# Kernel optimization log

Hardware: AMD Instinct MI355X
Metric: run time of the kernel (lower is better)

Reference implementation:

```python
import jax, jax.numpy as jnp
import numpy as np

N = 10000   # num_nodes
E = 320000  # num_edges (avg degree 32)
IN, HID, OUT = 512, 512, 256


def setup_inputs() -> dict:
    key = jax.random.key(0)
    ks = jax.random.split(key, 19)
    rn = lambda k, shape: (jax.random.normal(k, shape, jnp.float32) * 0.05)
    edge_index = jax.random.randint(ks[0], (2, E), 0, N, dtype=jnp.int32)
    return {
        "edge_index": edge_index,
        "w_pe": rn(ks[1], (IN, N)), "b_pe": rn(ks[2], (IN,)),
        "w_self0": rn(ks[3], (HID, IN)), "w_neigh0": rn(ks[4], (HID, IN)), "b0": rn(ks[5], (HID,)),
        "w_res0": rn(ks[6], (HID, IN)), "rb0": rn(ks[7], (HID,)),
        "w_self1": rn(ks[8], (HID, HID)), "w_neigh1": rn(ks[9], (HID, HID)), "b1": rn(ks[10], (HID,)),
        "w_res1": rn(ks[11], (HID, HID)), "rb1": rn(ks[12], (HID,)),
        "w_self2": rn(ks[13], (OUT, HID)), "w_neigh2": rn(ks[14], (OUT, HID)), "b2": rn(ks[15], (OUT,)),
        "w_res2": rn(ks[16], (OUT, HID)), "rb2": rn(ks[17], (OUT,)),
    }


def reference(edge_index, w_pe, b_pe,
              w_self0, w_neigh0, b0, w_res0, rb0,
              w_self1, w_neigh1, b1, w_res1, rb1,
              w_self2, w_neigh2, b2, w_res2, rb2):
    src, dst = edge_index[0], edge_index[1]

    def mean_agg(h):
        # mean of neighbor features per destination node (sparse SAGE aggregation)
        s = jax.ops.segment_sum(h[src], dst, num_segments=N)           # [N, D]
        deg = jax.ops.segment_sum(jnp.ones((E,), h.dtype), dst, num_segments=N)
        return s / jnp.maximum(deg, 1.0)[:, None]

    # pe = Linear(eye(N)) as in the original module
    pe = jnp.eye(N, dtype=w_pe.dtype) @ w_pe.T + b_pe                   # [N, IN]

    layers = [
        (w_self0, w_neigh0, b0, w_res0, rb0),
        (w_self1, w_neigh1, b1, w_res1, rb1),
        (w_self2, w_neigh2, b2, w_res2, rb2),
    ]

    h = pe
    mids = []
    for i, (ws, wn, b, wr, rb) in enumerate(layers):
        h_prev = h
        # SAGEConv (mean): fc_self(h) + fc_neigh(mean_neigh(h))
        h = h @ ws.T + mean_agg(h_prev) @ wn.T + b
        if i != len(layers) - 1:
            h = jax.nn.leaky_relu(h, 0.01)
            # F.dropout with training=False is identity (inference reference)
        h = h + (h_prev @ wr.T + rb)  # residual linear
        mids.append(h)
    return (h, *mids)
```

## Files before the change

### kernel.cpp

```cpp
#include <hip/hip_runtime.h>

#define N_NODES 10000
#define N_EDGES 320000
#define DIN 512
#define DHID 512
#define DOUT 256

typedef __bf16 bf16x8 __attribute__((ext_vector_type(8)));
typedef float f32x4 __attribute__((ext_vector_type(4)));
typedef unsigned short ushort_t;
typedef unsigned int uint_t;

__device__ __forceinline__ float b2f(ushort_t u){
    union { uint_t i; float f; } v; v.i = (uint_t)u << 16; return v.f;
}
__device__ __forceinline__ float blo(uint_t v){
    union { uint_t i; float f; } u; u.i = v << 16; return u.f;
}
__device__ __forceinline__ float bhi(uint_t v){
    union { uint_t i; float f; } u; u.i = v & 0xffff0000u; return u.f;
}
__device__ __forceinline__ ushort_t f2b(float f){
    union { float f; uint_t i; } v; v.f = f;
    uint_t i = v.i;
    return (ushort_t)((i + 0x7fffu + ((i >> 16) & 1u)) >> 16);
}

__device__ __forceinline__ void gll16(const ushort_t* g, ushort_t* l){
    __builtin_amdgcn_global_load_lds(
        (const __attribute__((address_space(1))) unsigned int*)g,
        (__attribute__((address_space(3))) unsigned int*)l,
        16, 0, 0);
}


__global__ void k_degree(const int* __restrict__ dst, int* __restrict__ deg){
    int e = blockIdx.x * 256 + threadIdx.x;
    if (e < N_EDGES) atomicAdd(&deg[dst[e]], 1);
}

__global__ void k_scan(const int* __restrict__ deg, int* __restrict__ row_ptr,
                       int* __restrict__ cursor){
    __shared__ int part[256];
    int t = threadIdx.x;
    int base = t * 40;
    int loc[40];
    int s = 0;
    #pragma unroll
    for (int i = 0; i < 40; ++i){
        int idx = base + i;
        int v = (idx < N_NODES) ? deg[idx] : 0;
        s += v; loc[i] = s;
    }
    part[t] = s;
    __syncthreads();
    int val = s;
    for (int off = 1; off < 256; off <<= 1){
        int x = (t >= off) ? part[t - off] : 0;
        __syncthreads();
        val += x; part[t] = val;
        __syncthreads();
    }
    int exc = val - s;
    if (t == 0) row_ptr[0] = 0;
    int run = exc;
    #pragma unroll
    for (int i = 0; i < 40; ++i){
        int idx = base + i;
        if (idx < N_NODES){
            row_ptr[idx + 1] = exc + loc[i];
            cursor[idx] = run;
        }
        run = exc + loc[i];
    }
}

__global__ void k_scatter(const int* __restrict__ src, const int* __restrict__ dst,
                          int* __restrict__ cursor, int* __restrict__ srcs){
    int e = blockIdx.x * 256 + threadIdx.x;
    if (e < N_EDGES){
        int p = atomicAdd(&cursor[dst[e]], 1);
        srcs[p] = src[e];
    }
}


struct CvtArgs { const float* s[8]; const float* s2[8]; ushort_t* d[8]; int n[8]; };

__global__ void k_pro(const float* __restrict__ w_pe, const float* __restrict__ b_pe,
                      ushort_t* __restrict__ h0, CvtArgs a,
                      int* __restrict__ deg, uint_t* __restrict__ zp){
    __shared__ float lt[64][68];
    int bid = blockIdx.x;
    int t = threadIdx.x;
    if (bid < 1256){
        int n0 = (bid % 157) * 64, i0 = (bid / 157) * 64;
        int nc = (t & 15) * 4, ir = t >> 4;
        #pragma unroll
        for (int p = 0; p < 4; ++p){
            int i_loc = ir + p * 16;
            float4 v = {0.f, 0.f, 0.f, 0.f};
            if (n0 + nc < N_NODES)
                v = *(const float4*)&w_pe[(size_t)(i0 + i_loc) * N_NODES + n0 + nc];
            lt[nc + 0][i_loc] = v.x;
            lt[nc + 1][i_loc] = v.y;
            lt[nc + 2][i_loc] = v.z;
            lt[nc + 3][i_loc] = v.w;
        }
        __syncthreads();
        int ic = t & 7, nr = t >> 3;
        #pragma unroll
        for (int p = 0; p < 2; ++p){
            int n_loc = nr + p * 32;
            int n = n0 + n_loc;
            if (n < N_NODES){
                uint4 u;
                u.x = (uint_t)f2b(lt[n_loc][ic*8+0] + b_pe[i0+ic*8+0])
                    | ((uint_t)f2b(lt[n_loc][ic*8+1] + b_pe[i0+ic*8+1]) << 16);
                u.y = (uint_t)f2b(lt[n_loc][ic*8+2] + b_pe[i0+ic*8+2])
                    | ((uint_t)f2b(lt[n_loc][ic*8+3] + b_pe[i0+ic*8+3]) << 16);
                u.z = (uint_t)f2b(lt[n_loc][ic*8+4] + b_pe[i0+ic*8+4])
                    | ((uint_t)f2b(lt[n_loc][ic*8+5] + b_pe[i0+ic*8+5]) << 16);
                u.w = (uint_t)f2b(lt[n_loc][ic*8+6] + b_pe[i0+ic*8+6])
                    | ((uint_t)f2b(lt[n_loc][ic*8+7] + b_pe[i0+ic*8+7]) << 16);
                *(uint4*)&h0[(size_t)n * DIN + i0 + ic * 8] = u;
            }
        }
    } else if (bid < 2280){
        int j = bid - 1256;
        int m = j >> 7;
        int i = (((j & 127) * 256) + t) * 8;
        if (i < a.n[m]){
            const float* sp = a.s[m] + i;
            float4 f0 = *(const float4*)sp;
            float4 f1 = *(const float4*)(sp + 4);
            if (a.s2[m]){
                const float* sq = a.s2[m] + i;
                float4 g0 = *(const float4*)sq;
                float4 g1 = *(const float4*)(sq + 4);
                f0.x += g0.x; f0.y += g0.y; f0.z += g0.z; f0.w += g0.w;
                f1.x += g1.x; f1.y += g1.y; f1.z += g1.z; f1.w += g1.w;
            }
            uint4 u;
            u.x = (uint_t)f2b(f0.x) | ((uint_t)f2b(f0.y) << 16);
            u.y = (uint_t)f2b(f0.z) | ((uint_t)f2b(f0.w) << 16);
            u.z = (uint_t)f2b(f1.x) | ((uint_t)f2b(f1.y) << 16);
            u.w = (uint_t)f2b(f1.z) | ((uint_t)f2b(f1.w) << 16);
            *(uint4*)&a.d[m][i] = u;
        }
    } else {
        int i = (bid - 2280) * 256 + t;
        if (i < N_NODES) deg[i] = 0;
        if (i < 256) zp[i] = 0u;
    }
}


#define AGG_EDGE(e, CH) { \
    int s_ = __builtin_amdgcn_readlane(sr, (e)); \
    uint_t v_ = *(const uint_t*)&X[((size_t)(uint_t)s_ << 9) + col]; \
    CH##0 += blo(v_); CH##1 += bhi(v_); }

__global__ __launch_bounds__(256) void k_agg(
    const ushort_t* __restrict__ X, const int* __restrict__ row_ptr,
    const int* __restrict__ srcs, ushort_t* __restrict__ out, int dummy)
{
    int w = threadIdx.x >> 6, lane = threadIdx.x & 63;
    int n = blockIdx.x * 4 + w;
    int col = blockIdx.y * 128 + lane * 2;
    int beg = row_ptr[n], end = row_ptr[n + 1];
    int deg = end - beg;
    float a0=0.f,a1=0.f, p0=0.f,p1=0.f, c0=0.f,c1=0.f, d0=0.f,d1=0.f;

    for (int base = beg; base < end; base += 64){
        int rem = end - base;
        int sr = (lane < rem) ? srcs[base + lane] : dummy;
        int cnt = rem < 64 ? rem : 64;
        #pragma unroll
        for (int k = 0; k < 4; ++k){
            if (k * 16 < cnt){
                int L = k * 16;
                AGG_EDGE(L + 0,  a) AGG_EDGE(L + 1,  p) AGG_EDGE(L + 2,  c) AGG_EDGE(L + 3,  d)
                AGG_EDGE(L + 4,  a) AGG_EDGE(L + 5,  p) AGG_EDGE(L + 6,  c) AGG_EDGE(L + 7,  d)
                AGG_EDGE(L + 8,  a) AGG_EDGE(L + 9,  p) AGG_EDGE(L + 10, c) AGG_EDGE(L + 11, d)
                AGG_EDGE(L + 12, a) AGG_EDGE(L + 13, p) AGG_EDGE(L + 14, c) AGG_EDGE(L + 15, d)
            }
        }
    }

    float r0 = (a0 + p0) + (c0 + d0);
    float r1 = (a1 + p1) + (c1 + d1);
    float inv = (deg > 0) ? 1.f / (float)deg : 1.f;
    uint_t o = (uint_t)f2b(r0 * inv) | ((uint_t)f2b(r1 * inv) << 16);
    *(uint_t*)&out[(size_t)n * 512 + col] = o;
}


#define AGGF_EDGE(e, CH) { \
    int s_ = __builtin_amdgcn_readlane(sr, (e)); \
    uint_t v_ = *(const uint_t*)&P[((size_t)(uint_t)s_ << 8) + col]; \
    CH##0 += blo(v_); CH##1 += bhi(v_); }

__global__ __launch_bounds__(256) void k_aggf(
    const ushort_t* __restrict__ P, const int* __restrict__ row_ptr,
    const int* __restrict__ srcs, const float* __restrict__ Q,
    float* __restrict__ fin, float* __restrict__ mid2, int dummy)
{
    int w = threadIdx.x >> 6, lane = threadIdx.x & 63;
    int n = blockIdx.x * 4 + w;
    int col = blockIdx.y * 128 + lane * 2;
    int beg = row_ptr[n], end = row_ptr[n + 1];
    int deg = end - beg;
    float a0=0.f,a1=0.f, p0=0.f,p1=0.f, c0=0.f,c1=0.f, d0=0.f,d1=0.f;

    for (int base = beg; base < end; base += 64){
        int rem = end - base;
        int sr = (lane < rem) ? srcs[base + lane] : dummy;
        int cnt = rem < 64 ? rem : 64;
        #pragma unroll
        for (int k = 0; k < 4; ++k){
            if (k * 16 < cnt){
                int L = k * 16;
                AGGF_EDGE(L + 0,  a) AGGF_EDGE(L + 1,  p) AGGF_EDGE(L + 2,  c) AGGF_EDGE(L + 3,  d)
                AGGF_EDGE(L + 4,  a) AGGF_EDGE(L + 5,  p) AGGF_EDGE(L + 6,  c) AGGF_EDGE(L + 7,  d)
                AGGF_EDGE(L + 8,  a) AGGF_EDGE(L + 9,  p) AGGF_EDGE(L + 10, c) AGGF_EDGE(L + 11, d)
                AGGF_EDGE(L + 12, a) AGGF_EDGE(L + 13, p) AGGF_EDGE(L + 14, c) AGGF_EDGE(L + 15, d)
            }
        }
    }

    float r0 = (a0 + p0) + (c0 + d0);
    float r1 = (a1 + p1) + (c1 + d1);
    float inv = (deg > 0) ? 1.f / (float)deg : 1.f;
    float2 q = *(const float2*)&Q[(size_t)n * 256 + col];
    float2 o;
    o.x = q.x + r0 * inv;
    o.y = q.y + r1 * inv;
    *(float2*)&fin [(size_t)n * 256 + col] = o;
    *(float2*)&mid2[(size_t)n * 256 + col] = o;
}


template<int DO, int BN, bool ACT, bool WRITE_BF>
__global__ __launch_bounds__(256, 2) void k_layer(
    const ushort_t* __restrict__ X, const ushort_t* __restrict__ G,
    const ushort_t* __restrict__ Ws, const ushort_t* __restrict__ Wn,
    const ushort_t* __restrict__ Wr,
    const float* __restrict__ b, const float* __restrict__ rb,
    float* __restrict__ Y, ushort_t* __restrict__ YB)
{
    constexpr int BM   = 160;
    constexpr int NT   = DO / BN;
    constexpr int WTN  = BN / 32;
    constexpr int NCH  = (2 * BM + 3 * BN) / 16;
    constexpr int CHPW = (NCH + 3) / 4;
    constexpr int OG   = BM * 32;
    constexpr int OS   = 2 * BM * 32;
    constexpr int WS32 = BN * 32;
    constexpr int BUFSZ = OS + 3 * WS32;
    __shared__ __align__(16) ushort_t smem[2][BUFSZ];

    int t = threadIdx.x;
    int bid = blockIdx.x;
    int r8 = bid & 7, q8 = bid >> 3;
    int m_t = (q8 / NT) * 8 + r8;
    int n_t = q8 % NT;
    if (m_t * BM >= N_NODES) return;
    int m0 = m_t * BM, n0 = n_t * BN;

    int lane = t & 63, w = t >> 6;
    int wr = w >> 1, wc = w & 1;

    const ushort_t* gptr[CHPW];
    int coff[CHPW];
    bool gv[CHPW];
    int rl = lane >> 2;
    int sl = ((lane & 3) ^ ((rl >> 1) & 3)) * 8;
    #pragma unroll
    for (int i = 0; i < CHPW; ++i){
        int qq = w * CHPW + i;
        gv[i] = (qq < NCH);
        int qc = gv[i] ? qq : 0;
        const ushort_t* gA; int rowbase, off;
        if (qc < 10)      { gA = X;  rowbase = m0 + qc * 16;        off = qc * 512; }
        else if (qc < 20) { gA = G;  rowbase = m0 + (qc - 10) * 16; off = OG + (qc - 10) * 512; }
        else {
            int q2 = qc - 20;
            int sec = q2 / (BN / 16), wi = q2 % (BN / 16);
            gA = (sec == 0) ? Ws : (sec == 1) ? Wn : Wr;
            rowbase = n0 + wi * 16;
            off = OS + sec * WS32 + wi * 512;
        }
        gptr[i] = gA + (size_t)(rowbase + rl) * 512 + sl;
        coff[i] = off;
    }

    f32x4 accS[5][WTN] = {}, accG[5][WTN] = {}, accR[5][WTN] = {};
    int r16 = lane & 15;
    int arow = wr * 80 + r16;
    int brow = wc * (BN / 2) + r16;
    int kk = ((lane >> 4) ^ ((r16 >> 1) & 3)) * 8;

    #pragma unroll
    for (int i = 0; i < CHPW; ++i) if (gv[i]) gll16(gptr[i], &smem[0][coff[i]]);
    __syncthreads();

    int cur = 0;
    for (int ks = 0; ks < 16; ++ks){
        if (ks < 15){
            int k0 = (ks + 1) * 32;
            #pragma unroll
            for (int i = 0; i < CHPW; ++i) if (gv[i]) gll16(gptr[i] + k0, &smem[cur ^ 1][coff[i]]);
        }

        const ushort_t* sb = smem[cur];
        bf16x8 ax[5], ag[5], bs[WTN], bn_[WTN], brr[WTN];
        #pragma unroll
        for (int m = 0; m < 5; ++m){
            ax[m] = *(const bf16x8*)&sb[(arow + m * 16) * 32 + kk];
            ag[m] = *(const bf16x8*)&sb[OG + (arow + m * 16) * 32 + kk];
        }
        #pragma unroll
        for (int n = 0; n < WTN; ++n){
            bs[n]  = *(const bf16x8*)&sb[OS            + (brow + n * 16) * 32 + kk];
            bn_[n] = *(const bf16x8*)&sb[OS + WS32     + (brow + n * 16) * 32 + kk];
            brr[n] = *(const bf16x8*)&sb[OS + 2 * WS32 + (brow + n * 16) * 32 + kk];
        }
        #pragma unroll
        for (int m = 0; m < 5; ++m)
            #pragma unroll
            for (int n = 0; n < WTN; ++n){
                accS[m][n] = __builtin_amdgcn_mfma_f32_16x16x32_bf16(ax[m], bs[n],  accS[m][n], 0, 0, 0);
                accG[m][n] = __builtin_amdgcn_mfma_f32_16x16x32_bf16(ag[m], bn_[n], accG[m][n], 0, 0, 0);
                accR[m][n] = __builtin_amdgcn_mfma_f32_16x16x32_bf16(ax[m], brr[n], accR[m][n], 0, 0, 0);
            }

        __syncthreads();
        cur ^= 1;
    }

    int col_l = lane & 15;
    int row_l = (lane >> 4) * 4;
    #pragma unroll
    for (int n = 0; n < WTN; ++n){
        int col = n0 + wc * (BN / 2) + n * 16 + col_l;
        float bb = b[col], rbb = rb[col];
        #pragma unroll
        for (int m = 0; m < 5; ++m){
            #pragma unroll
            for (int j = 0; j < 4; ++j){
                int row = m0 + wr * 80 + m * 16 + row_l + j;
                if (row < N_NODES){
                    float v = accS[m][n][j] + accG[m][n][j] + bb;
                    if (ACT) v = (v > 0.f) ? v : 0.01f * v;
                    v += accR[m][n][j] + rbb;
                    Y[(size_t)row * DO + col] = v;
                    if (WRITE_BF) YB[(size_t)row * DO + col] = f2b(v);
                }
            }
        }
    }
}


__global__ __launch_bounds__(256, 2) void k_layer2(
    const ushort_t* __restrict__ X,
    const ushort_t* __restrict__ Wn, const ushort_t* __restrict__ Wsr,
    const float* __restrict__ b, const float* __restrict__ rb,
    ushort_t* __restrict__ Pout, float* __restrict__ Qout)
{
    constexpr int BM = 160, BN = 32, NT = DOUT / BN;
    constexpr int NCH = 10 + 2 * (BN / 16);
    constexpr int CHPW = 4;
    constexpr int OWN = BM * 32;
    constexpr int OWS = OWN + BN * 32;
    constexpr int BUFSZ = OWS + BN * 32;
    __shared__ __align__(16) ushort_t smem[2][BUFSZ];

    int t = threadIdx.x;
    int bid = blockIdx.x;
    int r8 = bid & 7, q8 = bid >> 3;
    int m_t = (q8 / NT) * 8 + r8;
    int n_t = q8 % NT;
    if (m_t * BM >= N_NODES) return;
    int m0 = m_t * BM, n0 = n_t * BN;

    int lane = t & 63, w = t >> 6;
    int wr = w >> 1, wc = w & 1;

    const ushort_t* gptr[CHPW];
    int coff[CHPW];
    bool gv[CHPW];
    int rl = lane >> 2;
    int sl = ((lane & 3) ^ ((rl >> 1) & 3)) * 8;
    #pragma unroll
    for (int i = 0; i < CHPW; ++i){
        int qq = w * CHPW + i;
        gv[i] = (qq < NCH);
        int qc = gv[i] ? qq : 0;
        const ushort_t* gA; int rowbase, off;
        if (qc < 10)      { gA = X;   rowbase = m0 + qc * 16;        off = qc * 512; }
        else if (qc < 12) { gA = Wn;  rowbase = n0 + (qc - 10) * 16; off = OWN + (qc - 10) * 512; }
        else              { gA = Wsr; rowbase = n0 + (qc - 12) * 16; off = OWS + (qc - 12) * 512; }
        gptr[i] = gA + (size_t)(rowbase + rl) * 512 + sl;
        coff[i] = off;
    }

    f32x4 accP[5] = {}, accQ[5] = {};
    int r16 = lane & 15;
    int arow = wr * 80 + r16;
    int brow = wc * 16 + r16;
    int kk = ((lane >> 4) ^ ((r16 >> 1) & 3)) * 8;

    #pragma unroll
    for (int i = 0; i < CHPW; ++i) if (gv[i]) gll16(gptr[i], &smem[0][coff[i]]);
    __syncthreads();

    int cur = 0;
    for (int ks = 0; ks < 16; ++ks){
        if (ks < 15){
            int k0 = (ks + 1) * 32;
            #pragma unroll
            for (int i = 0; i < CHPW; ++i) if (gv[i]) gll16(gptr[i] + k0, &smem[cur ^ 1][coff[i]]);
        }

        const ushort_t* sb = smem[cur];
        bf16x8 ax[5];
        #pragma unroll
        for (int m = 0; m < 5; ++m)
            ax[m] = *(const bf16x8*)&sb[(arow + m * 16) * 32 + kk];
        bf16x8 bn_ = *(const bf16x8*)&sb[OWN + brow * 32 + kk];
        bf16x8 bsr = *(const bf16x8*)&sb[OWS + brow * 32 + kk];
        #pragma unroll
        for (int m = 0; m < 5; ++m){
            accP[m] = __builtin_amdgcn_mfma_f32_16x16x32_bf16(ax[m], bn_, accP[m], 0, 0, 0);
            accQ[m] = __builtin_amdgcn_mfma_f32_16x16x32_bf16(ax[m], bsr, accQ[m], 0, 0, 0);
        }

        __syncthreads();
        cur ^= 1;
    }

    int col_l = lane & 15;
    int row_l = (lane >> 4) * 4;
    int col = n0 + wc * 16 + col_l;
    float bb = b[col] + rb[col];
    #pragma unroll
    for (int m = 0; m < 5; ++m){
        #pragma unroll
        for (int j = 0; j < 4; ++j){
            int row = m0 + wr * 80 + m * 16 + row_l + j;
            if (row < N_NODES){
                Qout[(size_t)row * DOUT + col] = accQ[m][j] + bb;
                Pout[(size_t)row * DOUT + col] = f2b(accP[m][j]);
            }
        }
    }
}


extern "C" void kernel_launch(void* const* d_in, const int* in_sizes, int n_in,
                              void* d_out, int out_size, void* d_ws, size_t ws_size,
                              hipStream_t stream) {
    const int* edge  = (const int*)d_in[0];
    const int* e_src = edge;
    const int* e_dst = edge + N_EDGES;
    const float* w_pe = (const float*)d_in[1];
    const float* b_pe = (const float*)d_in[2];
    const float* ws0 = (const float*)d_in[3];
    const float* wn0 = (const float*)d_in[4];
    const float* b0  = (const float*)d_in[5];
    const float* wr0 = (const float*)d_in[6];
    const float* rb0 = (const float*)d_in[7];
    const float* ws1 = (const float*)d_in[8];
    const float* wn1 = (const float*)d_in[9];
    const float* b1  = (const float*)d_in[10];
    const float* wr1 = (const float*)d_in[11];
    const float* rb1 = (const float*)d_in[12];
    const float* ws2 = (const float*)d_in[13];
    const float* wn2 = (const float*)d_in[14];
    const float* b2  = (const float*)d_in[15];
    const float* wr2 = (const float*)d_in[16];
    const float* rb2 = (const float*)d_in[17];

    char* wsb = (char*)d_ws;
    ushort_t* h0   = (ushort_t*)wsb;
    ushort_t* hb   = (ushort_t*)(wsb + 10240000);
    ushort_t* aggb = (ushort_t*)(wsb + 20480000);
    ushort_t* wbf  = (ushort_t*)(wsb + 30720000);
    int* deg     = (int*)(wsb + 34652160);
    int* row_ptr = deg + 10016;
    int* cursor  = row_ptr + 10016;
    int* srcs    = cursor + 10016;
    uint_t* zp   = (uint_t*)(wsb + 36052992);
    const int dummy_h0 = 35208;
    const int dummy_hb = 25208;
    const int dummy_pb = 30416;

    ushort_t* wbf0s = wbf;
    ushort_t* wbf0n = wbf + 262144;
    ushort_t* wbf0r = wbf + 524288;
    ushort_t* wbf1s = wbf + 786432;
    ushort_t* wbf1n = wbf + 1048576;
    ushort_t* wbf1r = wbf + 1310720;
    ushort_t* wbf2n = wbf + 1572864;
    ushort_t* wbf2sr= wbf + 1703936;

    float* out  = (float*)d_out;
    float* fin  = out;
    float* mid0 = out + 2560000;
    float* mid1 = out + 7680000;
    float* mid2 = out + 12800000;
    ushort_t* pb = aggb;

    CvtArgs ca;
    ca.s[0]=ws0; ca.s[1]=wn0; ca.s[2]=wr0;
    ca.s[3]=ws1; ca.s[4]=wn1; ca.s[5]=wr1;
    ca.s[6]=wn2; ca.s[7]=ws2;
    for (int i = 0; i < 8; ++i) ca.s2[i] = nullptr;
    ca.s2[7] = wr2;
    ca.d[0]=wbf0s; ca.d[1]=wbf0n; ca.d[2]=wbf0r;
    ca.d[3]=wbf1s; ca.d[4]=wbf1n; ca.d[5]=wbf1r;
    ca.d[6]=wbf2n; ca.d[7]=wbf2sr;
    for (int i = 0; i < 6; ++i) ca.n[i] = 262144;
    ca.n[6] = 131072; ca.n[7] = 131072;

    k_pro<<<2320, 256, 0, stream>>>(w_pe, b_pe, h0, ca, deg, zp);

    k_degree <<<1250, 256, 0, stream>>>(e_dst, deg);
    k_scan   <<<1, 256, 0, stream>>>(deg, row_ptr, cursor);
    k_scatter<<<1250, 256, 0, stream>>>(e_src, e_dst, cursor, srcs);

    k_agg<<<dim3(2500, 4), 256, 0, stream>>>(h0, row_ptr, srcs, aggb, dummy_h0);
    k_layer<512, 64, true, true ><<<dim3(512), 256, 0, stream>>>(
        h0, aggb, wbf0s, wbf0n, wbf0r, b0, rb0, mid0, hb);

    k_agg<<<dim3(2500, 4), 256, 0, stream>>>(hb, row_ptr, srcs, aggb, dummy_hb);
    k_layer<512, 64, true, true ><<<dim3(512), 256, 0, stream>>>(
        hb, aggb, wbf1s, wbf1n, wbf1r, b1, rb1, mid1, h0);

    k_layer2<<<dim3(512), 256, 0, stream>>>(h0, wbf2n, wbf2sr, b2, rb2, pb, mid2);
    k_aggf<<<dim3(2500, 2), 256, 0, stream>>>(pb, row_ptr, srcs, mid2, fin, mid2, dummy_pb);
}
```

Measured before the change: 206.5 us.

## Merge prologue and CSR build into one cooperative kernel with grid syncs

Folds four front-end kernels (weight conversion and PE transpose, degree count, scan, scatter) into one persistent cooperative kernel of 1024 blocks. Grid-wide syncs separate the phases. The aim is to remove three kernel launch gaps and the tail drain between them. In exchange, the single-block scan phase now leaves the rest of the grid idle at a barrier, and a cooperative launch needs all 1024 blocks to be co-resident.

```diff
diff --git a/kernel.cpp b/kernel.cpp
--- a/kernel.cpp
+++ b/kernel.cpp
@@ -1,4 +1,7 @@
 #include <hip/hip_runtime.h>
+#include <hip/hip_cooperative_groups.h>
+
+namespace cg = cooperative_groups;
 
 #define N_NODES 10000
 #define N_EDGES 320000
@@ -34,124 +37,133 @@
 }
 
 
-__global__ void k_degree(const int* __restrict__ dst, int* __restrict__ deg){
-    int e = blockIdx.x * 256 + threadIdx.x;
-    if (e < N_EDGES) atomicAdd(&deg[dst[e]], 1);
-}
-
-__global__ void k_scan(const int* __restrict__ deg, int* __restrict__ row_ptr,
-                       int* __restrict__ cursor){
-    __shared__ int part[256];
+struct CvtArgs { const float* s[8]; const float* s2[8]; ushort_t* d[8]; int n[8]; };
+
+__global__ void k_front(const int* __restrict__ e_src, const int* __restrict__ e_dst,
+                        const float* __restrict__ w_pe, const float* __restrict__ b_pe,
+                        ushort_t* __restrict__ h0, CvtArgs a,
+                        int* __restrict__ deg, uint_t* __restrict__ zp,
+                        int* __restrict__ row_ptr, int* __restrict__ cursor,
+                        int* __restrict__ srcs){
+    cg::grid_group grid = cg::this_grid();
+    __shared__ float lt[64][68];
     int t = threadIdx.x;
-    int base = t * 40;
-    int loc[40];
-    int s = 0;
-    #pragma unroll
-    for (int i = 0; i < 40; ++i){
-        int idx = base + i;
-        int v = (idx < N_NODES) ? deg[idx] : 0;
-        s += v; loc[i] = s;
-    }
-    part[t] = s;
-    __syncthreads();
-    int val = s;
-    for (int off = 1; off < 256; off <<= 1){
-        int x = (t >= off) ? part[t - off] : 0;
+
+    for (int job = blockIdx.x; job < 2320; job += gridDim.x){
+        if (job < 1256){
+            int n0 = (job % 157) * 64, i0 = (job / 157) * 64;
+            int nc = (t & 15) * 4, ir = t >> 4;
+            #pragma unroll
+            for (int p = 0; p < 4; ++p){
+                int i_loc = ir + p * 16;
+                float4 v = {0.f, 0.f, 0.f, 0.f};
+                if (n0 + nc < N_NODES)
+                    v = *(const float4*)&w_pe[(size_t)(i0 + i_loc) * N_NODES + n0 + nc];
+                lt[nc + 0][i_loc] = v.x;
+                lt[nc + 1][i_loc] = v.y;
+                lt[nc + 2][i_loc] = v.z;
+                lt[nc + 3][i_loc] = v.w;
+            }
+            __syncthreads();
+            int ic = t & 7, nr = t >> 3;
+            #pragma unroll
+            for (int p = 0; p < 2; ++p){
+                int n_loc = nr + p * 32;
+                int n = n0 + n_loc;
+                if (n < N_NODES){
+                    uint4 u;
+                    u.x = (uint_t)f2b(lt[n_loc][ic*8+0] + b_pe[i0+ic*8+0])
+                        | ((uint_t)f2b(lt[n_loc][ic*8+1] + b_pe[i0+ic*8+1]) << 16);
+                    u.y = (uint_t)f2b(lt[n_loc][ic*8+2] + b_pe[i0+ic*8+2])
+                        | ((uint_t)f2b(lt[n_loc][ic*8+3] + b_pe[i0+ic*8+3]) << 16);
+                    u.z = (uint_t)f2b(lt[n_loc][ic*8+4] + b_pe[i0+ic*8+4])
+                        | ((uint_t)f2b(lt[n_loc][ic*8+5] + b_pe[i0+ic*8+5]) << 16);
+                    u.w = (uint_t)f2b(lt[n_loc][ic*8+6] + b_pe[i0+ic*8+6])
+                        | ((uint_t)f2b(lt[n_loc][ic*8+7] + b_pe[i0+ic*8+7]) << 16);
+                    *(uint4*)&h0[(size_t)n * DIN + i0 + ic * 8] = u;
+                }
+            }
+        } else if (job < 2280){
+            int j = job - 1256;
+            int m = j >> 7;
+            int i = (((j & 127) * 256) + t) * 8;
+            if (i < a.n[m]){
+                const float* sp = a.s[m] + i;
+                float4 f0 = *(const float4*)sp;
+                float4 f1 = *(const float4*)(sp + 4);
+                if (a.s2[m]){
+                    const float* sq = a.s2[m] + i;
+                    float4 g0 = *(const float4*)sq;
+                    float4 g1 = *(const float4*)(sq + 4);
+                    f0.x += g0.x; f0.y += g0.y; f0.z += g0.z; f0.w += g0.w;
+                    f1.x += g1.x; f1.y += g1.y; f1.z += g1.z; f1.w += g1.w;
+                }
+                uint4 u;
+                u.x = (uint_t)f2b(f0.x) | ((uint_t)f2b(f0.y) << 16);
+                u.y = (uint_t)f2b(f0.z) | ((uint_t)f2b(f0.w) << 16);
+                u.z = (uint_t)f2b(f1.x) | ((uint_t)f2b(f1.y) << 16);
+                u.w = (uint_t)f2b(f1.z) | ((uint_t)f2b(f1.w) << 16);
+                *(uint4*)&a.d[m][i] = u;
+            }
+        } else {
+            int i = (job - 2280) * 256 + t;
+            if (i < N_NODES) deg[i] = 0;
+            if (i < 256) zp[i] = 0u;
+        }
         __syncthreads();
-        val += x; part[t] = val;
+    }
+    __threadfence();
+    grid.sync();
+
+    for (int job = blockIdx.x; job < 1250; job += gridDim.x){
+        int e = job * 256 + t;
+        if (e < N_EDGES) atomicAdd(&deg[e_dst[e]], 1);
+    }
+    __threadfence();
+    grid.sync();
+
+    if (blockIdx.x == 0){
+        int* part = (int*)&lt[0][0];
+        int base = t * 40;
+        int loc[40];
+        int s = 0;
+        #pragma unroll
+        for (int i = 0; i < 40; ++i){
+            int idx = base + i;
+            int v = (idx < N_NODES) ? deg[idx] : 0;
+            s += v; loc[i] = s;
+        }
+        part[t] = s;
         __syncthreads();
-    }
-    int exc = val - s;
-    if (t == 0) row_ptr[0] = 0;
-    int run = exc;
-    #pragma unroll
-    for (int i = 0; i < 40; ++i){
-        int idx = base + i;
-        if (idx < N_NODES){
-            row_ptr[idx + 1] = exc + loc[i];
-            cursor[idx] = run;
-        }
-        run = exc + loc[i];
-    }
-}
-
-__global__ void k_scatter(const int* __restrict__ src, const int* __restrict__ dst,
-                          int* __restrict__ cursor, int* __restrict__ srcs){
-    int e = blockIdx.x * 256 + threadIdx.x;
-    if (e < N_EDGES){
-        int p = atomicAdd(&cursor[dst[e]], 1);
-        srcs[p] = src[e];
-    }
-}
-
-
-struct CvtArgs { const float* s[8]; const float* s2[8]; ushort_t* d[8]; int n[8]; };
-
-__global__ void k_pro(const float* __restrict__ w_pe, const float* __restrict__ b_pe,
-                      ushort_t* __restrict__ h0, CvtArgs a,
-                      int* __restrict__ deg, uint_t* __restrict__ zp){
-    __shared__ float lt[64][68];
-    int bid = blockIdx.x;
-    int t = threadIdx.x;
-    if (bid < 1256){
-        int n0 = (bid % 157) * 64, i0 = (bid / 157) * 64;
-        int nc = (t & 15) * 4, ir = t >> 4;
-        #pragma unroll
-        for (int p = 0; p < 4; ++p){
-            int i_loc = ir + p * 16;
-            float4 v = {0.f, 0.f, 0.f, 0.f};
-            if (n0 + nc < N_NODES)
-                v = *(const float4*)&w_pe[(size_t)(i0 + i_loc) * N_NODES + n0 + nc];
-            lt[nc + 0][i_loc] = v.x;
-            lt[nc + 1][i_loc] = v.y;
-            lt[nc + 2][i_loc] = v.z;
-            lt[nc + 3][i_loc] = v.w;
-        }
-        __syncthreads();
-        int ic = t & 7, nr = t >> 3;
-        #pragma unroll
-        for (int p = 0; p < 2; ++p){
-            int n_loc = nr + p * 32;
-            int n = n0 + n_loc;
-            if (n < N_NODES){
-                uint4 u;
-                u.x = (uint_t)f2b(lt[n_loc][ic*8+0] + b_pe[i0+ic*8+0])
-                    | ((uint_t)f2b(lt[n_loc][ic*8+1] + b_pe[i0+ic*8+1]) << 16);
-                u.y = (uint_t)f2b(lt[n_loc][ic*8+2] + b_pe[i0+ic*8+2])
-                    | ((uint_t)f2b(lt[n_loc][ic*8+3] + b_pe[i0+ic*8+3]) << 16);
-                u.z = (uint_t)f2b(lt[n_loc][ic*8+4] + b_pe[i0+ic*8+4])
-                    | ((uint_t)f2b(lt[n_loc][ic*8+5] + b_pe[i0+ic*8+5]) << 16);
-                u.w = (uint_t)f2b(lt[n_loc][ic*8+6] + b_pe[i0+ic*8+6])
-                    | ((uint_t)f2b(lt[n_loc][ic*8+7] + b_pe[i0+ic*8+7]) << 16);
-                *(uint4*)&h0[(size_t)n * DIN + i0 + ic * 8] = u;
-            }
-        }
-    } else if (bid < 2280){
-        int j = bid - 1256;
-        int m = j >> 7;
-        int i = (((j & 127) * 256) + t) * 8;
-        if (i < a.n[m]){
-            const float* sp = a.s[m] + i;
-            float4 f0 = *(const float4*)sp;
-            float4 f1 = *(const float4*)(sp + 4);
-            if (a.s2[m]){
-                const float* sq = a.s2[m] + i;
-                float4 g0 = *(const float4*)sq;
-                float4 g1 = *(const float4*)(sq + 4);
-                f0.x += g0.x; f0.y += g0.y; f0.z += g0.z; f0.w += g0.w;
-                f1.x += g1.x; f1.y += g1.y; f1.z += g1.z; f1.w += g1.w;
-            }
-            uint4 u;
-            u.x = (uint_t)f2b(f0.x) | ((uint_t)f2b(f0.y) << 16);
-            u.y = (uint_t)f2b(f0.z) | ((uint_t)f2b(f0.w) << 16);
-            u.z = (uint_t)f2b(f1.x) | ((uint_t)f2b(f1.y) << 16);
-            u.w = (uint_t)f2b(f1.z) | ((uint_t)f2b(f1.w) << 16);
-            *(uint4*)&a.d[m][i] = u;
-        }
-    } else {
-        int i = (bid - 2280) * 256 + t;
-        if (i < N_NODES) deg[i] = 0;
-        if (i < 256) zp[i] = 0u;
+        int val = s;
+        for (int off = 1; off < 256; off <<= 1){
+            int x = (t >= off) ? part[t - off] : 0;
+            __syncthreads();
+            val += x; part[t] = val;
+            __syncthreads();
+        }
+        int exc = val - s;
+        if (t == 0) row_ptr[0] = 0;
+        int run = exc;
+        #pragma unroll
+        for (int i = 0; i < 40; ++i){
+            int idx = base + i;
+            if (idx < N_NODES){
+                row_ptr[idx + 1] = exc + loc[i];
+                cursor[idx] = run;
+            }
+            run = exc + loc[i];
+        }
+    }
+    __threadfence();
+    grid.sync();
+
+    for (int job = blockIdx.x; job < 1250; job += gridDim.x){
+        int e = job * 256 + t;
+        if (e < N_EDGES){
+            int p = atomicAdd(&cursor[e_dst[e]], 1);
+            srcs[p] = e_src[e];
+        }
     }
 }
 
@@ -525,11 +537,15 @@
     for (int i = 0; i < 6; ++i) ca.n[i] = 262144;
     ca.n[6] = 131072; ca.n[7] = 131072;
 
-    k_pro<<<2320, 256, 0, stream>>>(w_pe, b_pe, h0, ca, deg, zp);
-
-    k_degree <<<1250, 256, 0, stream>>>(e_dst, deg);
-    k_scan   <<<1, 256, 0, stream>>>(deg, row_ptr, cursor);
-    k_scatter<<<1250, 256, 0, stream>>>(e_src, e_dst, cursor, srcs);
+    {
+        void* args[] = {
+            (void*)&e_src, (void*)&e_dst, (void*)&w_pe, (void*)&b_pe,
+            (void*)&h0, (void*)&ca, (void*)&deg, (void*)&zp,
+            (void*)&row_ptr, (void*)&cursor, (void*)&srcs
+        };
+        hipLaunchCooperativeKernel((const void*)k_front, dim3(1024), dim3(256),
+                                   args, 0, stream);
+    }
 
     k_agg<<<dim3(2500, 4), 256, 0, stream>>>(h0, row_ptr, srcs, aggb, dummy_h0);
     k_layer<512, 64, true, true ><<<dim3(512), 256, 0, stream>>>(
```

After: 728.8 us. +253.0%, slower.
